# Performance work log

Measured on AMD Instinct MI355X. Metric: run time of the kernel, lower is better.

## Reference

```python
import jax, jax.numpy as jnp
import numpy as np
from jax.scipy.linalg import cholesky, solve_triangular, cho_solve

N, M, D = 16384, 2048, 8
VAR, LS = 1.0, 0.5      # RBF kernel hyperparameters (same for kernel_f and kernel_g)
JITTER = 1e-6
BATCH_RATE = 1.0
HALF_LOG_2PI = 0.5 * float(np.log(2.0 * np.pi))


def rbf(x1, x2):
    # K[i,j] = VAR * exp(-||x1_i - x2_j||^2 / (2 LS^2))
    d2 = (jnp.sum(x1 * x1, 1)[:, None] + jnp.sum(x2 * x2, 1)[None, :]
          - 2.0 * (x1 @ x2.T))
    return VAR * jnp.exp(-0.5 * d2 / (LS * LS))


def setup_inputs() -> dict:
    key = jax.random.key(0)
    ks = jax.random.split(key, 7)
    x = jax.random.normal(ks[0], (N, D), dtype=jnp.float32)
    y = jax.random.normal(ks[1], (N, 1), dtype=jnp.float32)
    z = 2.0 * jax.random.uniform(ks[2], (M, D), dtype=jnp.float32) - 1.0  # inducing inputs in [-1,1]^D
    q_m_f = 0.5 * jax.random.normal(ks[3], (M, 1), dtype=jnp.float32)
    q_m_g = 0.5 * jax.random.normal(ks[4], (M, 1), dtype=jnp.float32)
    # Cholesky-like params: identity plus small strictly-lower noise -> PD covariance
    q_L_f = jnp.eye(M, dtype=jnp.float32) + 0.01 * jnp.tril(
        jax.random.normal(ks[5], (M, M), dtype=jnp.float32), -1)
    q_L_g = jnp.eye(M, dtype=jnp.float32) + 0.01 * jnp.tril(
        jax.random.normal(ks[6], (M, M), dtype=jnp.float32), -1)
    return {"x": x, "y": y, "z": z, "q_m_f": q_m_f, "q_L_f": q_L_f,
            "q_m_g": q_m_g, "q_L_g": q_L_g}


def _gp_marginals_and_kl(x, z, q_m, q_L_raw):
    """Marginal posterior mean/var at x and KL(q(u)||p(u)) for one sparse GP."""
    L_S = jnp.tril(q_L_raw)                     # [M,M]
    Kuu = rbf(z, z) + JITTER * jnp.eye(M, dtype=x.dtype)
    Lk = cholesky(Kuu, lower=True)
    Kfu = rbf(x, z)                             # [N,M]
    # A = Kfu @ Kuu^{-1}
    A = cho_solve((Lk, True), Kfu.T).T          # [N,M]
    m = (A @ q_m)[:, 0]                         # [N]
    # diag(Kff + A (S - Kuu) A^T) = diag(Kff) + diag(A S A^T) - diag(Kfu A^T)
    S = L_S @ L_S.T
    diag_Kff = jnp.full((x.shape[0],), VAR, dtype=x.dtype)
    v = diag_Kff + jnp.sum((A @ S) * A, axis=1) - jnp.sum(A * Kfu, axis=1)
    # KL(N(q_m, S) || N(0, Kuu))
    alpha = solve_triangular(Lk, q_m, lower=True)       # Kuu^{-1/2} m
    W = solve_triangular(Lk, L_S, lower=True)           # Kuu^{-1/2} L_S
    logdet_K = 2.0 * jnp.sum(jnp.log(jnp.diag(Lk)))
    logdet_S = 2.0 * jnp.sum(jnp.log(jnp.abs(jnp.diag(L_S))))
    kl = 0.5 * (jnp.sum(W * W) + jnp.sum(alpha * alpha)
                - jnp.asarray(M, x.dtype) + logdet_K - logdet_S)
    return m, v, kl


def reference(x, y, z, q_m_f, q_L_f, q_m_g, q_L_g):
    m_f, v_f, kl_f = _gp_marginals_and_kl(x, z, q_m_f, q_L_f)
    m_g, v_g, kl_g = _gp_marginals_and_kl(x, z, q_m_g, q_L_g)
    yv = y[:, 0]
    # HetGaussian variational expectation (Saul et al. 2016):
    # E_q[log N(y | f, exp(g))] per point
    expectation = (-HALF_LOG_2PI - 0.5 * m_g
                   - 0.5 * ((yv - m_f) ** 2 + v_f) * jnp.exp(-m_g + 0.5 * v_g))
    elbo = BATCH_RATE * jnp.sum(expectation) - (kl_f + kl_g)
    return -elbo
```

## Files before the change

kernel.cpp:

```cpp
#include <hip/hip_runtime.h>
#include <math.h>

#define NN 16384
#define MM 2048
#define DD 8
#define NB 32
#define GRIDN 512
#define SZB ((size_t)16777216)

constexpr float HLOG2PI = 0.91893853320467274178f;

using short8  = __attribute__((ext_vector_type(8))) short;
using float4v = __attribute__((ext_vector_type(4))) float;

__device__ __forceinline__ float4v f4zero(){ float4v v; v[0]=0.f; v[1]=0.f; v[2]=0.f; v[3]=0.f; return v; }

__device__ __forceinline__ void bfsplit(float v, short& h, short& lo){
  unsigned b = __float_as_uint(v);
  h = (short)(b >> 16);
  float hf = __uint_as_float(b & 0xFFFF0000u);
  lo = (short)(__float_as_uint(v - hf) >> 16);
}
__device__ __forceinline__ float bf2f(short s){
  return __uint_as_float(((unsigned)(unsigned short)s) << 16);
}
__device__ __forceinline__ float4v mfma3(short8 ah, short8 al, short8 bh, short8 bl, float4v c){
  c = __builtin_amdgcn_mfma_f32_16x16x32_bf16(ah, bh, c, 0, 0, 0);
  c = __builtin_amdgcn_mfma_f32_16x16x32_bf16(ah, bl, c, 0, 0, 0);
  c = __builtin_amdgcn_mfma_f32_16x16x32_bf16(al, bh, c, 0, 0, 0);
  return c;
}

__device__ __forceinline__ void gbar0(int* cnt, int* flag, int& gen){
  __syncthreads();
  if (threadIdx.x == 0){
    ++gen;
    __builtin_amdgcn_fence(__ATOMIC_RELEASE, "agent");
    int old = __hip_atomic_fetch_add(cnt, 1, __ATOMIC_RELAXED, __HIP_MEMORY_SCOPE_AGENT);
    if (old == gen*GRIDN - 1){
      __builtin_amdgcn_fence(__ATOMIC_ACQ_REL, "agent");
      __hip_atomic_store(flag, gen, __ATOMIC_RELAXED, __HIP_MEMORY_SCOPE_AGENT);
    } else {
      while (__hip_atomic_load(flag, __ATOMIC_RELAXED, __HIP_MEMORY_SCOPE_AGENT) < gen)
        __builtin_amdgcn_s_sleep(8);
    }
    __builtin_amdgcn_fence(__ATOMIC_ACQUIRE, "agent");
  }
  __syncthreads();
}

__device__ __forceinline__ void gbar_h(int* bar, int xcc, int myN, int nxcd, int& gen){
  __syncthreads();
  if (threadIdx.x == 0){
    ++gen;
    int* lcnt  = bar + xcc*32;
    int* lflag = bar + 512 + xcc*32;
    int* gcnt  = bar + 1024;
    int* gflag = bar + 1056;
    int old = __hip_atomic_fetch_add(lcnt, 1, __ATOMIC_RELAXED, __HIP_MEMORY_SCOPE_AGENT);
    if (old == gen*myN - 1){
      __builtin_amdgcn_fence(__ATOMIC_RELEASE, "agent");
      int g = __hip_atomic_fetch_add(gcnt, 1, __ATOMIC_RELAXED, __HIP_MEMORY_SCOPE_AGENT);
      if (g == gen*nxcd - 1){
        __hip_atomic_store(gflag, gen, __ATOMIC_RELAXED, __HIP_MEMORY_SCOPE_AGENT);
      } else {
        while (__hip_atomic_load(gflag, __ATOMIC_RELAXED, __HIP_MEMORY_SCOPE_AGENT) < gen)
          __builtin_amdgcn_s_sleep(8);
      }
      __builtin_amdgcn_fence(__ATOMIC_ACQUIRE, "agent");
      __hip_atomic_store(lflag, gen, __ATOMIC_RELAXED, __HIP_MEMORY_SCOPE_AGENT);
    } else {
      while (__hip_atomic_load(lflag, __ATOMIC_RELAXED, __HIP_MEMORY_SCOPE_AGENT) < gen)
        __builtin_amdgcn_s_sleep(8);
      __builtin_amdgcn_fence(__ATOMIC_ACQUIRE, "agent");
    }
  }
  __syncthreads();
}

__device__ __forceinline__ float block_reduce(float v, float* scratch){
  int lane = threadIdx.x & 63;
  int w    = threadIdx.x >> 6;
  #pragma unroll
  for (int off=32; off; off>>=1) v += __shfl_down(v, off, 64);
  __syncthreads();
  if (lane==0) scratch[w] = v;
  __syncthreads();
  float r = 0.f;
  if (threadIdx.x < 4) r = scratch[threadIdx.x];
  if (w==0){ r += __shfl_down(r, 2, 64); r += __shfl_down(r, 1, 64); }
  return r;
}

__device__ __forceinline__ void stage64(float (*S)[68], const float* __restrict__ g, int ld, int t){
  #pragma unroll
  for (int p=t; p<1024; p+=256)
    *(float4*)&S[p>>4][(p&15)*4] = *(const float4*)&g[(size_t)(p>>4)*ld + (p&15)*4];
}
__device__ __forceinline__ void tile_gemm_step(float acc[4][4], const float (*As)[68], const float (*Bs)[68], int tx, int ty){
  for (int k=0;k<64;++k){
    float ar[4], bc4[4];
    #pragma unroll
    for (int u=0;u<4;++u){ ar[u]=As[ty*4+u][k]; bc4[u]=Bs[k][tx*4+u]; }
    #pragma unroll
    for (int u=0;u<4;++u)
      #pragma unroll
      for (int v=0;v<4;++v) acc[u][v] += ar[u]*bc4[v];
  }
}
__device__ __forceinline__ void tile_syrk_step(float acc[4][4], const float (*P)[68], const float (*Q)[68], int tx, int ty){
  for (int k=0;k<64;++k){
    float pr[4], qc[4];
    #pragma unroll
    for (int u=0;u<4;++u){ pr[u]=P[ty*4+u][k]; qc[u]=Q[tx*4+u][k]; }
    #pragma unroll
    for (int u=0;u<4;++u)
      #pragma unroll
      for (int v=0;v<4;++v) acc[u][v] += pr[u]*qc[v];
  }
}

__device__ __forceinline__ void factor64_reg(const float (*S)[68],
    float* __restrict__ lkd, float* __restrict__ sdg_, int d, int t){
  if (t < 64){
    float xr[64];
    #pragma unroll
    for (int c4=0;c4<16;++c4) *(float4*)&xr[c4*4] = *(const float4*)&S[t][c4*4];
    float myrp = 1.f;
    #pragma unroll
    for (int j=0;j<64;++j){
      float ajj = __shfl(xr[j], j, 64);
      float piv = sqrtf(fmaxf(ajj, 1e-20f));
      float rp  = 1.f/piv;
      float val = xr[j]*rp;
      if (t==j){ xr[j] = piv; myrp = rp; }
      else if (t>j) xr[j] = val;
      else val = 0.f;
      #pragma unroll
      for (int c=j+1;c<64;++c){
        float vc = __shfl(val, c, 64);
        if (c<=t) xr[c] -= val*vc;
      }
    }
    #pragma unroll
    for (int c=0;c<64;++c) if (c>t) xr[c] = 0.f;
    #pragma unroll
    for (int c4=0;c4<16;++c4)
      *(float4*)&lkd[d*4096 + t*64 + c4*4] = *(float4*)&xr[c4*4];
    sdg_[d*64 + t] = myrp;
  }
}

__global__ __launch_bounds__(256, 2) void factor_coop(
    const float* __restrict__ z,
    const float* __restrict__ qlf, const float* __restrict__ qlg,
    const float* __restrict__ qmf, const float* __restrict__ qmg,
    float* __restrict__ kuu, float* __restrict__ linv,
    float* __restrict__ wf, float* __restrict__ wg,
    float* __restrict__ af, float* __restrict__ ag,
    float* __restrict__ ptmp, float* __restrict__ lkdiag,
    float* __restrict__ sdg, float* __restrict__ ltri, int* __restrict__ bar)
{
  __shared__ float As[64][68];
  __shared__ float Bs[64][68];
  __shared__ float Cs[64][68];
  __shared__ float sd[64];
  __shared__ int binfo[2];
  const int bid = blockIdx.x, t = threadIdx.x;
  const int tx = t & 15, ty = t >> 4;

  int xcc_r;
  asm volatile("s_getreg_b32 %0, hwreg(HW_REG_XCC_ID)" : "=s"(xcc_r));
  const int xcc = xcc_r & 15;
  if (t == 0)
    __hip_atomic_fetch_add(bar + 1152 + xcc*32, 1, __ATOMIC_RELAXED, __HIP_MEMORY_SCOPE_AGENT);
  int gen0 = 0;
  gbar0(bar + 1088, bar + 1120, gen0);
  if (t == 0){
    int myN = __hip_atomic_load(bar + 1152 + xcc*32, __ATOMIC_RELAXED, __HIP_MEMORY_SCOPE_AGENT);
    int nx = 0;
    for (int i=0;i<16;++i)
      nx += (__hip_atomic_load(bar + 1152 + i*32, __ATOMIC_RELAXED, __HIP_MEMORY_SCOPE_AGENT) > 0);
    binfo[0] = myN; binfo[1] = nx;
  }
  __syncthreads();
  const int myN = binfo[0], nxcd = binfo[1];
  int gen = 0;

  if (bid == 0){
    for (int p=t; p<128; p+=256){ int i=p>>1, h=p&1;
      *(float4*)&As[i][h*4] = *(const float4*)&z[(size_t)i*DD + h*4]; }
    __syncthreads();
    float kv[4][4];
    #pragma unroll
    for (int u=0;u<4;++u)
      #pragma unroll
      for (int v=0;v<4;++v){
        float d2=0.f;
        #pragma unroll
        for (int d=0;d<8;++d){ float df=As[ty*4+u][d]-As[tx*4+v][d]; d2+=df*df; }
        kv[u][v] = __expf(-2.f*d2) + ((ty*4+u)==(tx*4+v) ? 1e-6f : 0.f);
      }
    __syncthreads();
    #pragma unroll
    for (int u=0;u<4;++u)
      #pragma unroll
      for (int v=0;v<4;++v) As[ty*4+u][tx*4+v] = kv[u][v];
    __syncthreads();
    factor64_reg(As, lkdiag, sdg, 0, t);
  } else {
    for (int idx=bid; idx<528; idx+=GRIDN-1){
      int r=0; while ((r+1)*(r+2)/2 <= idx) ++r;
      int c = idx - r*(r+1)/2;
      __syncthreads();
      for (int p=t; p<128; p+=256){ int i=p>>1, h=p&1;
        *(float4*)&As[i][h*4] = *(const float4*)&z[(size_t)(r*64+i)*DD + h*4];
        *(float4*)&Bs[i][h*4] = *(const float4*)&z[(size_t)(c*64+i)*DD + h*4]; }
      __syncthreads();
      #pragma unroll
      for (int u=0;u<4;++u){
        float4 o;
        float* ov = (float*)&o;
        #pragma unroll
        for (int v=0;v<4;++v){
          float d2=0.f;
          #pragma unroll
          for (int d=0;d<8;++d){ float df=As[ty*4+u][d]-Bs[tx*4+v][d]; d2+=df*df; }
          float val = __expf(-2.f*d2);
          if (r*64+ty*4+u == c*64+tx*4+v) val += 1e-6f;
          ov[v] = val;
        }
        *(float4*)&kuu[(size_t)(r*64+ty*4+u)*MM + c*64 + tx*4] = o;
      }
    }
  }
  gbar_h(bar, xcc, myN, nxcd, gen);

  for (int kb=0; kb<31; ++kb){
    int T = NB-1 - kb;
    int ntiles = T*(T+1)/2;
    if (bid < ntiles){
      stage64(Cs, lkdiag + kb*4096, 64, t);
      if (t < 64) sd[t] = sdg[kb*64 + t];
    }
    for (int idx=bid; idx<ntiles; idx+=GRIDN){
      int r=0; while ((r+1)*(r+2)/2 <= idx) ++r;
      int c = idx - r*(r+1)/2;
      int bi = kb+1+r, bc = kb+1+c;
      __syncthreads();
      stage64(As, kuu + (size_t)(bi*64)*MM + kb*64, MM, t);
      if (bc != bi) stage64(Bs, kuu + (size_t)(bc*64)*MM + kb*64, MM, t);
      __syncthreads();
      {
        int w = t>>6, l = t&63;
        if (w==0 || (w==1 && bc!=bi)){
          float (*S)[68] = (w==0)? As : Bs;
          float xr[64];
          #pragma unroll
          for (int c4=0;c4<16;++c4) *(float4*)&xr[c4*4] = *(const float4*)&S[l][c4*4];
          #pragma unroll
          for (int j=0;j<64;++j){
            float xj = xr[j]*sd[j];
            xr[j] = xj;
            #pragma unroll
            for (int cc=j+1;cc<64;++cc) xr[cc] -= xj*Cs[cc][j];
          }
          #pragma unroll
          for (int c4=0;c4<16;++c4) *(float4*)&S[l][c4*4] = *(float4*)&xr[c4*4];
        }
      }
      __syncthreads();
      if (bc == kb+1){
        for (int p=t;p<1024;p+=256)
          *(float4*)&ltri[(size_t)(bi*64+(p>>4))*MM + kb*64 + (p&15)*4] =
              *(float4*)&As[p>>4][(p&15)*4];
      }
      float acc[4][4] = {};
      tile_syrk_step(acc, As, (bc==bi)? As : Bs, tx, ty);
      if (bi==kb+1 && bc==kb+1){
        __syncthreads();
        #pragma unroll
        for (int u=0;u<4;++u)
          #pragma unroll
          for (int v=0;v<4;++v) Bs[ty*4+u][tx*4+v] = acc[u][v];
        __syncthreads();
        for (int p=t;p<1024;p+=256){
          int i=p>>4, c4=p&15;
          float4 kv = *(const float4*)&kuu[(size_t)(bi*64+i)*MM + bi*64 + c4*4];
          float4 bv = *(float4*)&Bs[i][c4*4];
          float4 o; o.x=kv.x-bv.x; o.y=kv.y-bv.y; o.z=kv.z-bv.z; o.w=kv.w-bv.w;
          *(float4*)&As[i][c4*4] = o;
        }
        __syncthreads();
        factor64_reg(As, lkdiag, sdg, kb+1, t);
      } else {
        #pragma unroll
        for (int u=0;u<4;++u){
          float4* dst = (float4*)&kuu[(size_t)(bi*64+ty*4+u)*MM + bc*64 + tx*4];
          float4 o = *dst;
          o.x-=acc[u][0]; o.y-=acc[u][1]; o.z-=acc[u][2]; o.w-=acc[u][3];
          *dst = o;
        }
      }
    }
    gbar_h(bar, xcc, myN, nxcd, gen);
  }

  if (bid < NB){
    stage64(As, lkdiag + bid*4096, 64, t);
    __syncthreads();
    if (t < 64){
      for (int j=0;j<64;++j){
        float s = (j==t)?1.f:0.f;
        for (int k=t;k<j;++k) s -= As[j][k]*Bs[k][t];
        Bs[j][t] = (j>=t)? s/As[j][j] : 0.f;
      }
    }
    __syncthreads();
    for (int p=t;p<1024;p+=256){ int i=p>>4, c4=p&15;
      *(float4*)&linv[(size_t)(bid*64+i)*MM + bid*64 + c4*4] = *(float4*)&Bs[i][c4*4]; }
  }
  gbar_h(bar, xcc, myN, nxcd, gen);

  for (int idx=bid; idx<16; idx+=GRIDN){
    int m = idx;
    __syncthreads();
    stage64(As, ltri + (size_t)((2*m+1)*64)*MM + (2*m)*64, MM, t);
    stage64(Bs, linv + (size_t)((2*m)*64)*MM   + (2*m)*64, MM, t);
    __syncthreads();
    float acc[4][4]={};
    tile_gemm_step(acc, As, Bs, tx, ty);
    __syncthreads();
    #pragma unroll
    for (int u=0;u<4;++u)
      #pragma unroll
      for (int v=0;v<4;++v) Bs[ty*4+u][tx*4+v] = acc[u][v];
    stage64(As, linv + (size_t)((2*m+1)*64)*MM + (2*m+1)*64, MM, t);
    __syncthreads();
    float o[4][4]={};
    tile_gemm_step(o, As, Bs, tx, ty);
    #pragma unroll
    for (int u=0;u<4;++u)
      *(float4*)&linv[(size_t)((2*m+1)*64+ty*4+u)*MM + (2*m)*64 + tx*4] =
          make_float4(-o[u][0],-o[u][1],-o[u][2],-o[u][3]);
  }
  gbar_h(bar, xcc, myN, nxcd, gen);

  for (int m=bid; m<8; m+=GRIDN){
    float* pm = ptmp + (size_t)m*128*128;
    for (int ti=0; ti<2; ++ti)
      for (int tj=0; tj<2; ++tj){
        int rb = m*4 + 2 + ti, cb0 = m*4;
        float acc[4][4]={};
        for (int k=tj; k<2; ++k){
          __syncthreads();
          stage64(As, ltri + (size_t)(rb*64)*MM + (cb0+k)*64, MM, t);
          stage64(Bs, linv + (size_t)((cb0+k)*64)*MM + (cb0+tj)*64, MM, t);
          __syncthreads();
          tile_gemm_step(acc, As, Bs, tx, ty);
        }
        #pragma unroll
        for (int u=0;u<4;++u)
          *(float4*)&pm[(size_t)(ti*64+ty*4+u)*128 + tj*64 + tx*4] =
              make_float4(acc[u][0],acc[u][1],acc[u][2],acc[u][3]);
      }
    for (int ti=0; ti<2; ++ti)
      for (int tj=0; tj<2; ++tj){
        int rb = m*4 + 2 + ti;
        float acc[4][4]={};
        for (int k=0; k<=ti; ++k){
          __syncthreads();
          stage64(As, linv + (size_t)(rb*64)*MM + (m*4+2+k)*64, MM, t);
          stage64(Bs, pm + (size_t)(k*64)*128 + tj*64, 128, t);
          __syncthreads();
          tile_gemm_step(acc, As, Bs, tx, ty);
        }
        #pragma unroll
        for (int u=0;u<4;++u)
          *(float4*)&linv[(size_t)(rb*64+ty*4+u)*MM + (m*4+tj)*64 + tx*4] =
              make_float4(-acc[u][0],-acc[u][1],-acc[u][2],-acc[u][3]);
      }
  }
  gbar_h(bar, xcc, myN, nxcd, gen);

  for (int s=2; s<5; ++s){
    int nb = 1<<s, mc = 16>>s, b = 64<<s;
    float* pmb = ptmp + (s==2 ? 131072 : (s==3 ? 393216 : 917504));
    int tiles = mc*nb*nb;
    for (int idx=bid; idx<tiles; idx+=GRIDN){
      int m = idx/(nb*nb), r2 = idx%(nb*nb);
      int ti = r2/nb, tj = r2%nb;
      int rb = m*2*nb + nb + ti, cb0 = m*2*nb;
      float acc[4][4]={};
      for (int k=tj; k<nb; ++k){
        __syncthreads();
        stage64(As, ltri + (size_t)(rb*64)*MM + (cb0+k)*64, MM, t);
        stage64(Bs, linv + (size_t)((cb0+k)*64)*MM + (cb0+tj)*64, MM, t);
        __syncthreads();
        tile_gemm_step(acc, As, Bs, tx, ty);
      }
      float* pm = pmb + (size_t)m*b*b;
      #pragma unroll
      for (int u=0;u<4;++u)
        *(float4*)&pm[(size_t)(ti*64+ty*4+u)*b + tj*64 + tx*4] =
            make_float4(acc[u][0],acc[u][1],acc[u][2],acc[u][3]);
    }
    gbar_h(bar, xcc, myN, nxcd, gen);
    for (int idx=bid; idx<tiles; idx+=GRIDN){
      int m = idx/(nb*nb), r2 = idx%(nb*nb);
      int ti = r2/nb, tj = r2%nb;
      int rb = m*2*nb + nb + ti;
      const float* pm = pmb + (size_t)m*b*b;
      float acc[4][4]={};
      for (int k=0; k<=ti; ++k){
        __syncthreads();
        stage64(As, linv + (size_t)(rb*64)*MM + (m*2*nb+nb+k)*64, MM, t);
        stage64(Bs, pm + (size_t)(k*64)*b + tj*64, b, t);
        __syncthreads();
        tile_gemm_step(acc, As, Bs, tx, ty);
      }
      #pragma unroll
      for (int u=0;u<4;++u)
        *(float4*)&linv[(size_t)(rb*64+ty*4+u)*MM + (m*2*nb+tj)*64 + tx*4] =
            make_float4(-acc[u][0],-acc[u][1],-acc[u][2],-acc[u][3]);
    }
    gbar_h(bar, xcc, myN, nxcd, gen);
  }

  for (int idx=bid; idx<2*528; idx+=GRIDN){
    int gp = idx/528, rem = idx%528;
    int bi=0; while ((bi+1)*(bi+2)/2 <= rem) ++bi;
    int bj = rem - bi*(bi+1)/2;
    const float* ql = gp ? qlg : qlf;
    float* w        = gp ? wg  : wf;
    float acc[4][4]={};
    for (int bk=bj; bk<=bi; ++bk){
      __syncthreads();
      stage64(As, linv + (size_t)(bi*64)*MM + bk*64, MM, t);
      stage64(Bs, ql   + (size_t)(bk*64)*MM + bj*64, MM, t);
      __syncthreads();
      if (bk==bj){
        for (int p=t;p<4096;p+=256){ int i=p>>6, c=p&63; if (i<c) Bs[i][c]=0.f; }
        __syncthreads();
      }
      tile_gemm_step(acc, As, Bs, tx, ty);
    }
    #pragma unroll
    for (int u=0;u<4;++u)
      *(float4*)&w[(size_t)(bi*64+ty*4+u)*MM + bj*64 + tx*4] =
          make_float4(acc[u][0],acc[u][1],acc[u][2],acc[u][3]);
  }
  {
    int gw = bid*4 + (t>>6), l = t&63;
    for (int job=gw; job<4096; job+=GRIDN*4){
      int gp = job>>11, r = job&2047;
      const float* qm = gp ? qmg : qmf;
      float s=0.f;
      for (int c=l; c<=r; c+=64) s += linv[(size_t)r*MM+c]*qm[c];
      #pragma unroll
      for (int off=32; off; off>>=1) s += __shfl_down(s, off, 64);
      if (l==0) (gp ? ag : af)[r] = s;
    }
  }
}


__global__ __launch_bounds__(256) void zfrag_kernel(const float* __restrict__ z,
    short* __restrict__ zfh, short* __restrict__ zfl, float* __restrict__ zn2){
  int zr = blockIdx.x*256 + threadIdx.x;
  float v[DD]; float s = 0.f;
  #pragma unroll
  for (int d=0; d<DD; ++d){ v[d] = z[zr*DD + d]; s += v[d]*v[d]; }
  zn2[zr] = s;
  size_t base = (size_t)(zr >> 4)*512 + (zr & 15)*32;
  #pragma unroll
  for (int k=0; k<32; ++k){
    short h = 0, lo = 0;
    if (k < DD) bfsplit(v[k], h, lo);
    zfh[base + k] = h; zfl[base + k] = lo;
  }
}

__global__ __launch_bounds__(256) void red_small(const float* __restrict__ lkd,
    const float* __restrict__ qlf, const float* __restrict__ qlg,
    const float* __restrict__ af, const float* __restrict__ ag,
    float* __restrict__ scal){
  __shared__ float scratch[4];
  float ldk=0, ldf=0, ldg=0, a2f=0, a2g=0;
  for (int i=threadIdx.x;i<MM;i+=256){
    int kb = i>>6, r = i&63;
    ldk += __logf(lkd[kb*4096 + r*64 + r]);
    ldf += __logf(fabsf(qlf[(size_t)i*MM+i]));
    ldg += __logf(fabsf(qlg[(size_t)i*MM+i]));
    float v = af[i]; a2f += v*v;
    v = ag[i];       a2g += v*v;
  }
  float r;
  r = block_reduce(ldk, scratch); if (threadIdx.x==0) scal[0] = 2.f*r;
  r = block_reduce(ldf, scratch); if (threadIdx.x==0) scal[1] = 2.f*r;
  r = block_reduce(ldg, scratch); if (threadIdx.x==0) scal[2] = 2.f*r;
  r = block_reduce(a2f, scratch); if (threadIdx.x==0) scal[3] = r;
  r = block_reduce(a2g, scratch); if (threadIdx.x==0) scal[4] = r;
}

__global__ __launch_bounds__(256) void redw_kernel(const float* __restrict__ wf,
    const float* __restrict__ wg, float* __restrict__ scal){
  __shared__ float scratch[4];
  size_t start  = (size_t)blockIdx.x*256 + threadIdx.x;
  size_t stride = (size_t)gridDim.x*256;
  float sf=0, sg=0;
  for (size_t p=start;p<(size_t)MM*MM;p+=stride){
    float v=wf[p]; sf += v*v;
    v=wg[p];       sg += v*v;
  }
  float r = block_reduce(sf, scratch);
  if (threadIdx.x==0) atomicAdd(&scal[5], r);
  r = block_reduce(sg, scratch);
  if (threadIdx.x==0) atomicAdd(&scal[6], r);
}

__global__ void kl_kernel(const float* __restrict__ scal, float* __restrict__ out){
  float klf = 0.5f*(scal[5] + scal[3] - (float)MM + scal[0] - scal[1]);
  float klg = 0.5f*(scal[6] + scal[4] - (float)MM + scal[0] - scal[2]);
  out[0] += klf + klg;
}

__global__ __launch_bounds__(256) void split_rowmajor(const float* __restrict__ src,
    short* __restrict__ dh, short* __restrict__ dl){
  int p = blockIdx.x*256 + threadIdx.x;
  int chunk = p >> 9, wi = p & 511;
  int mo = chunk >> 6, ko = chunk & 63;
  int row = mo*16 + (wi >> 5), col = ko*32 + (wi & 31);
  float v = src[(size_t)row*MM + col];
  short h, lo; bfsplit(v, h, lo);
  dh[p] = h; dl[p] = lo;
}

__global__ __launch_bounds__(256) void split_transpose(const float* __restrict__ src,
    short* __restrict__ dh, short* __restrict__ dl){
  __shared__ float tile[32][33];
  int t = threadIdx.x;
  int mb = blockIdx.x, kb = blockIdx.y;
  #pragma unroll
  for (int k=0;k<4;++k){
    int idx = t + k*256;
// ... 220 lines not shown
        bh[tm] = *(const short8*)&lBh[off];
        bl[tm] = *(const short8*)&lBl[off];
      }
      #pragma unroll
      for (int tn=0; tn<4; ++tn)
        #pragma unroll
        for (int tm=0; tm<4; ++tm)
          acc[tn][tm] = mfma3(ah[tn], al[tn], bh[tm], bl[tm], acc[tn][tm]);
    }
  }
  float rs[16];
  #pragma unroll
  for (int tn=0; tn<4; ++tn)
    #pragma unroll
    for (int r=0; r<4; ++r){
      float s = 0.f;
      #pragma unroll
      for (int tm=0; tm<4; ++tm){ float v = acc[tn][tm][r]; s += v*v; }
      rs[tn*4+r] = s;
    }
  #pragma unroll
  for (int off=8; off; off>>=1)
    #pragma unroll
    for (int k=0; k<16; ++k) rs[k] += __shfl_down(rs[k], off, 16);
  if (li == 0){
    #pragma unroll
    for (int tn=0; tn<4; ++tn)
      #pragma unroll
      for (int r=0; r<4; ++r){
        int n = istrip*128 + (w>>1)*64 + tn*16 + q*4 + r;
        atomicAdd(&vq[n], rs[tn*4+r]);
      }
  }
}

__global__ __launch_bounds__(256) void final_kernel(const float* __restrict__ y,
    const float* __restrict__ t2, const float* __restrict__ lf, const float* __restrict__ lg,
    const float* __restrict__ vfq, const float* __restrict__ vgq, float* __restrict__ out){
  __shared__ float scratch[4];
  int i = blockIdx.x*256 + threadIdx.x;
  float mf = lf[i], mg = lg[i];
  float vf = 1.f + vfq[i] - t2[i];
  float vg = 1.f + vgq[i] - t2[i];
  float dy = y[i] - mf;
  float e = -HLOG2PI - 0.5f*mg - 0.5f*(dy*dy + vf)*__expf(-mg + 0.5f*vg);
  float r = block_reduce(e, scratch);
  if (threadIdx.x==0) atomicAdd(out, -r);
}

extern "C" void kernel_launch(void* const* d_in, const int* in_sizes, int n_in,
                              void* d_out, int out_size, void* d_ws, size_t ws_size,
                              hipStream_t stream){
  (void)in_sizes; (void)n_in; (void)out_size; (void)ws_size;
  const float* x   = (const float*)d_in[0];
  const float* y   = (const float*)d_in[1];
  const float* z   = (const float*)d_in[2];
  const float* qmf = (const float*)d_in[3];
  const float* qlf = (const float*)d_in[4];
  const float* qmg = (const float*)d_in[5];
  const float* qlg = (const float*)d_in[6];
  float* out = (float*)d_out;
  char* Bw = (char*)d_ws;

  float* kuu  = (float*)Bw;
  float* linv = (float*)(Bw + SZB);
  float* wf   = (float*)(Bw + 2*SZB);
  float* wg   = (float*)(Bw + 3*SZB);
  short* lvh  = (short*)Bw;
  short* lvl  = (short*)(Bw + SZB/2);
  short* wfh  = (short*)(Bw + SZB);
  short* wfl  = (short*)(Bw + SZB + SZB/2);
  short* wgh  = (short*)(Bw + 2*SZB);
  short* wgl  = (short*)(Bw + 2*SZB + SZB/2);
  short* tth  = (short*)(Bw + 3*SZB);
  short* ttl  = (short*)(Bw + 3*SZB + (size_t)NN*MM*2);
  float* ltri   = (float*)(Bw + 4*SZB);
  float* ptmp   = (float*)(Bw + 5*SZB);
  float* lkdiag = (float*)(Bw + 5*SZB + (size_t)8388608);
  float* sdg    = (float*)(Bw + 5*SZB + (size_t)8388608 + (size_t)524288);
  float* sm   = (float*)(Bw + 3*SZB + (size_t)NN*MM*4);
  float* af = sm;          float* ag = af + MM;
  float* t2 = ag + MM;     float* lf = t2 + NN;   float* lg = lf + NN;
  float* vfq = lg + NN;    float* vgq = vfq + NN; float* scal = vgq + NN;
  int*   bar = (int*)(scal + 64);
  float* zn2 = scal + 64 + 2048;
  short* zfh = (short*)(zn2 + MM);
  short* zfl = zfh + MM*32;

  hipMemsetAsync(out, 0, sizeof(float), stream);
  hipMemsetAsync(vfq, 0, (size_t)(2*NN + 64 + 2048)*sizeof(float), stream);
  hipMemsetAsync(wf,  0, 2*SZB, stream);
  hipMemsetAsync(linv,0, SZB,   stream);

  zfrag_kernel<<<MM/256, 256, 0, stream>>>(z, zfh, zfl, zn2);

  factor_coop<<<GRIDN, 256, 0, stream>>>(z, qlf, qlg, qmf, qmg,
                                         kuu, linv, wf, wg, af, ag,
                                         ptmp, lkdiag, sdg, ltri, bar);

  red_small<<<1, 256, 0, stream>>>(lkdiag, qlf, qlg, af, ag, scal);
  redw_kernel<<<512, 256, 0, stream>>>(wf, wg, scal);
  kl_kernel<<<1, 1, 0, stream>>>(scal, out);

  split_rowmajor<<<MM*MM/256, 256, 0, stream>>>(linv, lvh, lvl);
  split_transpose<<<dim3(MM/32, MM/32), 256, 0, stream>>>(wf, wfh, wfl);
  split_transpose<<<dim3(MM/32, MM/32), 256, 0, stream>>>(wg, wgh, wgl);

  tt_mfma<<<dim3(NN/128, MM/128), 256, 0, stream>>>(x, zn2, zfh, zfl, lvh, lvl, tth, ttl);
  lin_v2<<<NN/4, 256, 0, stream>>>(tth, ttl, af, ag, t2, lf, lg);
  quad_mfma<<<dim3(NN/128, MM/128, 2), 256, 0, stream>>>(tth, ttl, wfh, wfl, wgh, wgl, vfq, vgq);
  final_kernel<<<NN/256, 256, 0, stream>>>(y, t2, lf, lg, vfq, vgq, out);
}
```

Measured before the change: 4.600 ms.

## Replace persistent cooperative factor kernel with per-phase kernel launches

Measured after the change: 3.914 ms. -14.9%, faster.

```diff
diff --git a/kernel.cpp b/kernel.cpp
--- a/kernel.cpp
+++ b/kernel.cpp
@@ -5,7 +5,6 @@
 #define MM 2048
 #define DD 8
 #define NB 32
-#define GRIDN 512
 #define SZB ((size_t)16777216)
 
 constexpr float HLOG2PI = 0.91893853320467274178f;
@@ -29,53 +28,6 @@
   c = __builtin_amdgcn_mfma_f32_16x16x32_bf16(ah, bl, c, 0, 0, 0);
   c = __builtin_amdgcn_mfma_f32_16x16x32_bf16(al, bh, c, 0, 0, 0);
   return c;
-}
-
-__device__ __forceinline__ void gbar0(int* cnt, int* flag, int& gen){
-  __syncthreads();
-  if (threadIdx.x == 0){
-    ++gen;
-    __builtin_amdgcn_fence(__ATOMIC_RELEASE, "agent");
-    int old = __hip_atomic_fetch_add(cnt, 1, __ATOMIC_RELAXED, __HIP_MEMORY_SCOPE_AGENT);
-    if (old == gen*GRIDN - 1){
-      __builtin_amdgcn_fence(__ATOMIC_ACQ_REL, "agent");
-      __hip_atomic_store(flag, gen, __ATOMIC_RELAXED, __HIP_MEMORY_SCOPE_AGENT);
-    } else {
-      while (__hip_atomic_load(flag, __ATOMIC_RELAXED, __HIP_MEMORY_SCOPE_AGENT) < gen)
-        __builtin_amdgcn_s_sleep(8);
-    }
-    __builtin_amdgcn_fence(__ATOMIC_ACQUIRE, "agent");
-  }
-  __syncthreads();
-}
-
-__device__ __forceinline__ void gbar_h(int* bar, int xcc, int myN, int nxcd, int& gen){
-  __syncthreads();
-  if (threadIdx.x == 0){
-    ++gen;
-    int* lcnt  = bar + xcc*32;
-    int* lflag = bar + 512 + xcc*32;
-    int* gcnt  = bar + 1024;
-    int* gflag = bar + 1056;
-    int old = __hip_atomic_fetch_add(lcnt, 1, __ATOMIC_RELAXED, __HIP_MEMORY_SCOPE_AGENT);
-    if (old == gen*myN - 1){
-      __builtin_amdgcn_fence(__ATOMIC_RELEASE, "agent");
-      int g = __hip_atomic_fetch_add(gcnt, 1, __ATOMIC_RELAXED, __HIP_MEMORY_SCOPE_AGENT);
-      if (g == gen*nxcd - 1){
-        __hip_atomic_store(gflag, gen, __ATOMIC_RELAXED, __HIP_MEMORY_SCOPE_AGENT);
-      } else {
-        while (__hip_atomic_load(gflag, __ATOMIC_RELAXED, __HIP_MEMORY_SCOPE_AGENT) < gen)
-          __builtin_amdgcn_s_sleep(8);
-      }
-      __builtin_amdgcn_fence(__ATOMIC_ACQUIRE, "agent");
-      __hip_atomic_store(lflag, gen, __ATOMIC_RELAXED, __HIP_MEMORY_SCOPE_AGENT);
-    } else {
-      while (__hip_atomic_load(lflag, __ATOMIC_RELAXED, __HIP_MEMORY_SCOPE_AGENT) < gen)
-        __builtin_amdgcn_s_sleep(8);
-      __builtin_amdgcn_fence(__ATOMIC_ACQUIRE, "agent");
-    }
-  }
-  __syncthreads();
 }
 
 __device__ __forceinline__ float block_reduce(float v, float* scratch){
@@ -151,316 +103,297 @@
   }
 }
 
-__global__ __launch_bounds__(256, 2) void factor_coop(
-    const float* __restrict__ z,
-    const float* __restrict__ qlf, const float* __restrict__ qlg,
-    const float* __restrict__ qmf, const float* __restrict__ qmg,
-    float* __restrict__ kuu, float* __restrict__ linv,
-    float* __restrict__ wf, float* __restrict__ wg,
-    float* __restrict__ af, float* __restrict__ ag,
-    float* __restrict__ ptmp, float* __restrict__ lkdiag,
-    float* __restrict__ sdg, float* __restrict__ ltri, int* __restrict__ bar)
-{
+
+__global__ __launch_bounds__(256) void phase0_kernel(
+    const float* __restrict__ z, float* __restrict__ kuu){
+  __shared__ float As[64][68];
+  __shared__ float Bs[64][68];
+  const int t = threadIdx.x, tx = t & 15, ty = t >> 4;
+  int idx = blockIdx.x;
+  int r=0; while ((r+1)*(r+2)/2 <= idx) ++r;
+  int c = idx - r*(r+1)/2;
+  for (int p=t; p<128; p+=256){ int i=p>>1, h=p&1;
+    *(float4*)&As[i][h*4] = *(const float4*)&z[(size_t)(r*64+i)*DD + h*4];
+    *(float4*)&Bs[i][h*4] = *(const float4*)&z[(size_t)(c*64+i)*DD + h*4]; }
+  __syncthreads();
+  #pragma unroll
+  for (int u=0;u<4;++u){
+    float4 o;
+    float* ov = (float*)&o;
+    #pragma unroll
+    for (int v=0;v<4;++v){
+      float d2=0.f;
+      #pragma unroll
+      for (int d=0;d<8;++d){ float df=As[ty*4+u][d]-Bs[tx*4+v][d]; d2+=df*df; }
+      float val = __expf(-2.f*d2);
+      if (r*64+ty*4+u == c*64+tx*4+v) val += 1e-6f;
+      ov[v] = val;
+    }
+    *(float4*)&kuu[(size_t)(r*64+ty*4+u)*MM + c*64 + tx*4] = o;
+  }
+}
+
+__global__ __launch_bounds__(256) void diag0_kernel(
+    const float* __restrict__ kuu, float* __restrict__ lkdiag, float* __restrict__ sdg){
+  __shared__ float As[64][68];
+  const int t = threadIdx.x;
+  stage64(As, kuu, MM, t);
+  __syncthreads();
+  factor64_reg(As, lkdiag, sdg, 0, t);
+}
+
+__global__ __launch_bounds__(256) void panel_kernel(
+    float* __restrict__ kuu, float* __restrict__ lkdiag,
+    float* __restrict__ sdg, float* __restrict__ ltri, int kb){
   __shared__ float As[64][68];
   __shared__ float Bs[64][68];
   __shared__ float Cs[64][68];
   __shared__ float sd[64];
-  __shared__ int binfo[2];
-  const int bid = blockIdx.x, t = threadIdx.x;
-  const int tx = t & 15, ty = t >> 4;
-
-  int xcc_r;
-  asm volatile("s_getreg_b32 %0, hwreg(HW_REG_XCC_ID)" : "=s"(xcc_r));
-  const int xcc = xcc_r & 15;
-  if (t == 0)
-    __hip_atomic_fetch_add(bar + 1152 + xcc*32, 1, __ATOMIC_RELAXED, __HIP_MEMORY_SCOPE_AGENT);
-  int gen0 = 0;
-  gbar0(bar + 1088, bar + 1120, gen0);
-  if (t == 0){
-    int myN = __hip_atomic_load(bar + 1152 + xcc*32, __ATOMIC_RELAXED, __HIP_MEMORY_SCOPE_AGENT);
-    int nx = 0;
-    for (int i=0;i<16;++i)
-      nx += (__hip_atomic_load(bar + 1152 + i*32, __ATOMIC_RELAXED, __HIP_MEMORY_SCOPE_AGENT) > 0);
-    binfo[0] = myN; binfo[1] = nx;
-  }
-  __syncthreads();
-  const int myN = binfo[0], nxcd = binfo[1];
-  int gen = 0;
-
-  if (bid == 0){
-    for (int p=t; p<128; p+=256){ int i=p>>1, h=p&1;
-      *(float4*)&As[i][h*4] = *(const float4*)&z[(size_t)i*DD + h*4]; }
-    __syncthreads();
-    float kv[4][4];
+  const int t = threadIdx.x, tx = t & 15, ty = t >> 4;
+  int idx = blockIdx.x;
+  int r=0; while ((r+1)*(r+2)/2 <= idx) ++r;
+  int c = idx - r*(r+1)/2;
+  int bi = kb+1+r, bc = kb+1+c;
+  stage64(Cs, lkdiag + kb*4096, 64, t);
+  if (t < 64) sd[t] = sdg[kb*64 + t];
+  stage64(As, kuu + (size_t)(bi*64)*MM + kb*64, MM, t);
+  if (bc != bi) stage64(Bs, kuu + (size_t)(bc*64)*MM + kb*64, MM, t);
+  __syncthreads();
+  {
+    int w = t>>6, l = t&63;
+    if (w==0 || (w==1 && bc!=bi)){
+      float (*S)[68] = (w==0)? As : Bs;
+      float xr[64];
+      #pragma unroll
+      for (int c4=0;c4<16;++c4) *(float4*)&xr[c4*4] = *(const float4*)&S[l][c4*4];
+      #pragma unroll
+      for (int j=0;j<64;++j){
+        float xj = xr[j]*sd[j];
+        xr[j] = xj;
+        #pragma unroll
+        for (int cc=j+1;cc<64;++cc) xr[cc] -= xj*Cs[cc][j];
+      }
+      #pragma unroll
+      for (int c4=0;c4<16;++c4) *(float4*)&S[l][c4*4] = *(float4*)&xr[c4*4];
+    }
+  }
+  __syncthreads();
+  if (bc == kb+1){
+    for (int p=t;p<1024;p+=256)
+      *(float4*)&ltri[(size_t)(bi*64+(p>>4))*MM + kb*64 + (p&15)*4] =
+          *(float4*)&As[p>>4][(p&15)*4];
+  }
+  float acc[4][4] = {};
+  tile_syrk_step(acc, As, (bc==bi)? As : Bs, tx, ty);
+  if (bi==kb+1 && bc==kb+1){
+    __syncthreads();
     #pragma unroll
     for (int u=0;u<4;++u)
       #pragma unroll
-      for (int v=0;v<4;++v){
-        float d2=0.f;
-        #pragma unroll
-        for (int d=0;d<8;++d){ float df=As[ty*4+u][d]-As[tx*4+v][d]; d2+=df*df; }
-        kv[u][v] = __expf(-2.f*d2) + ((ty*4+u)==(tx*4+v) ? 1e-6f : 0.f);
-      }
-    __syncthreads();
-    #pragma unroll
-    for (int u=0;u<4;++u)
-      #pragma unroll
-      for (int v=0;v<4;++v) As[ty*4+u][tx*4+v] = kv[u][v];
-    __syncthreads();
-    factor64_reg(As, lkdiag, sdg, 0, t);
+      for (int v=0;v<4;++v) Bs[ty*4+u][tx*4+v] = acc[u][v];
+    __syncthreads();
+    for (int p=t;p<1024;p+=256){
+      int i=p>>4, c4=p&15;
+      float4 kv = *(const float4*)&kuu[(size_t)(bi*64+i)*MM + bi*64 + c4*4];
+      float4 bv = *(float4*)&Bs[i][c4*4];
+      float4 o; o.x=kv.x-bv.x; o.y=kv.y-bv.y; o.z=kv.z-bv.z; o.w=kv.w-bv.w;
+      *(float4*)&As[i][c4*4] = o;
+    }
+    __syncthreads();
+    factor64_reg(As, lkdiag, sdg, kb+1, t);
   } else {
-    for (int idx=bid; idx<528; idx+=GRIDN-1){
-      int r=0; while ((r+1)*(r+2)/2 <= idx) ++r;
-      int c = idx - r*(r+1)/2;
-      __syncthreads();
-      for (int p=t; p<128; p+=256){ int i=p>>1, h=p&1;
-        *(float4*)&As[i][h*4] = *(const float4*)&z[(size_t)(r*64+i)*DD + h*4];
-        *(float4*)&Bs[i][h*4] = *(const float4*)&z[(size_t)(c*64+i)*DD + h*4]; }
-      __syncthreads();
-      #pragma unroll
-      for (int u=0;u<4;++u){
-        float4 o;
-        float* ov = (float*)&o;
-        #pragma unroll
-        for (int v=0;v<4;++v){
-          float d2=0.f;
-          #pragma unroll
-          for (int d=0;d<8;++d){ float df=As[ty*4+u][d]-Bs[tx*4+v][d]; d2+=df*df; }
-          float val = __expf(-2.f*d2);
-          if (r*64+ty*4+u == c*64+tx*4+v) val += 1e-6f;
-          ov[v] = val;
-        }
-        *(float4*)&kuu[(size_t)(r*64+ty*4+u)*MM + c*64 + tx*4] = o;
-      }
-    }
-  }
-  gbar_h(bar, xcc, myN, nxcd, gen);
-
-  for (int kb=0; kb<31; ++kb){
-    int T = NB-1 - kb;
-    int ntiles = T*(T+1)/2;
-    if (bid < ntiles){
-      stage64(Cs, lkdiag + kb*4096, 64, t);
-      if (t < 64) sd[t] = sdg[kb*64 + t];
-    }
-    for (int idx=bid; idx<ntiles; idx+=GRIDN){
-      int r=0; while ((r+1)*(r+2)/2 <= idx) ++r;
-      int c = idx - r*(r+1)/2;
-      int bi = kb+1+r, bc = kb+1+c;
-      __syncthreads();
-      stage64(As, kuu + (size_t)(bi*64)*MM + kb*64, MM, t);
-      if (bc != bi) stage64(Bs, kuu + (size_t)(bc*64)*MM + kb*64, MM, t);
-      __syncthreads();
-      {
-        int w = t>>6, l = t&63;
-        if (w==0 || (w==1 && bc!=bi)){
-          float (*S)[68] = (w==0)? As : Bs;
-          float xr[64];
-          #pragma unroll
-          for (int c4=0;c4<16;++c4) *(float4*)&xr[c4*4] = *(const float4*)&S[l][c4*4];
-          #pragma unroll
-          for (int j=0;j<64;++j){
-            float xj = xr[j]*sd[j];
-            xr[j] = xj;
-            #pragma unroll
-            for (int cc=j+1;cc<64;++cc) xr[cc] -= xj*Cs[cc][j];
-          }
-          #pragma unroll
-          for (int c4=0;c4<16;++c4) *(float4*)&S[l][c4*4] = *(float4*)&xr[c4*4];
-        }
-      }
-      __syncthreads();
-      if (bc == kb+1){
-        for (int p=t;p<1024;p+=256)
-          *(float4*)&ltri[(size_t)(bi*64+(p>>4))*MM + kb*64 + (p&15)*4] =
-              *(float4*)&As[p>>4][(p&15)*4];
-      }
-      float acc[4][4] = {};
-      tile_syrk_step(acc, As, (bc==bi)? As : Bs, tx, ty);
-      if (bi==kb+1 && bc==kb+1){
-        __syncthreads();
-        #pragma unroll
-        for (int u=0;u<4;++u)
-          #pragma unroll
-          for (int v=0;v<4;++v) Bs[ty*4+u][tx*4+v] = acc[u][v];
-        __syncthreads();
-        for (int p=t;p<1024;p+=256){
-          int i=p>>4, c4=p&15;
-          float4 kv = *(const float4*)&kuu[(size_t)(bi*64+i)*MM + bi*64 + c4*4];
-          float4 bv = *(float4*)&Bs[i][c4*4];
-          float4 o; o.x=kv.x-bv.x; o.y=kv.y-bv.y; o.z=kv.z-bv.z; o.w=kv.w-bv.w;
-          *(float4*)&As[i][c4*4] = o;
-        }
-        __syncthreads();
-        factor64_reg(As, lkdiag, sdg, kb+1, t);
-      } else {
-        #pragma unroll
-        for (int u=0;u<4;++u){
-          float4* dst = (float4*)&kuu[(size_t)(bi*64+ty*4+u)*MM + bc*64 + tx*4];
-          float4 o = *dst;
-          o.x-=acc[u][0]; o.y-=acc[u][1]; o.z-=acc[u][2]; o.w-=acc[u][3];
-          *dst = o;
-        }
-      }
-    }
-    gbar_h(bar, xcc, myN, nxcd, gen);
-  }
-
-  if (bid < NB){
-    stage64(As, lkdiag + bid*4096, 64, t);
-    __syncthreads();
-    if (t < 64){
-      for (int j=0;j<64;++j){
-        float s = (j==t)?1.f:0.f;
-        for (int k=t;k<j;++k) s -= As[j][k]*Bs[k][t];
-        Bs[j][t] = (j>=t)? s/As[j][j] : 0.f;
-      }
-    }
-    __syncthreads();
-    for (int p=t;p<1024;p+=256){ int i=p>>4, c4=p&15;
-      *(float4*)&linv[(size_t)(bid*64+i)*MM + bid*64 + c4*4] = *(float4*)&Bs[i][c4*4]; }
-  }
-  gbar_h(bar, xcc, myN, nxcd, gen);
-
-  for (int idx=bid; idx<16; idx+=GRIDN){
-    int m = idx;
-    __syncthreads();
-    stage64(As, ltri + (size_t)((2*m+1)*64)*MM + (2*m)*64, MM, t);
-    stage64(Bs, linv + (size_t)((2*m)*64)*MM   + (2*m)*64, MM, t);
-    __syncthreads();
-    float acc[4][4]={};
-    tile_gemm_step(acc, As, Bs, tx, ty);
-    __syncthreads();
-    #pragma unroll
-    for (int u=0;u<4;++u)
-      #pragma unroll
-      for (int v=0;v<4;++v) Bs[ty*4+u][tx*4+v] = acc[u][v];
-    stage64(As, linv + (size_t)((2*m+1)*64)*MM + (2*m+1)*64, MM, t);
-    __syncthreads();
-    float o[4][4]={};
-    tile_gemm_step(o, As, Bs, tx, ty);
-    #pragma unroll
-    for (int u=0;u<4;++u)
-      *(float4*)&linv[(size_t)((2*m+1)*64+ty*4+u)*MM + (2*m)*64 + tx*4] =
-          make_float4(-o[u][0],-o[u][1],-o[u][2],-o[u][3]);
-  }
-  gbar_h(bar, xcc, myN, nxcd, gen);
-
-  for (int m=bid; m<8; m+=GRIDN){
-    float* pm = ptmp + (size_t)m*128*128;
-    for (int ti=0; ti<2; ++ti)
-      for (int tj=0; tj<2; ++tj){
-        int rb = m*4 + 2 + ti, cb0 = m*4;
-        float acc[4][4]={};
-        for (int k=tj; k<2; ++k){
-          __syncthreads();
-          stage64(As, ltri + (size_t)(rb*64)*MM + (cb0+k)*64, MM, t);
-          stage64(Bs, linv + (size_t)((cb0+k)*64)*MM + (cb0+tj)*64, MM, t);
-          __syncthreads();
-          tile_gemm_step(acc, As, Bs, tx, ty);
-        }
-        #pragma unroll
-        for (int u=0;u<4;++u)
-          *(float4*)&pm[(size_t)(ti*64+ty*4+u)*128 + tj*64 + tx*4] =
-              make_float4(acc[u][0],acc[u][1],acc[u][2],acc[u][3]);
-      }
-    for (int ti=0; ti<2; ++ti)
-      for (int tj=0; tj<2; ++tj){
-        int rb = m*4 + 2 + ti;
-        float acc[4][4]={};
-        for (int k=0; k<=ti; ++k){
-          __syncthreads();
-          stage64(As, linv + (size_t)(rb*64)*MM + (m*4+2+k)*64, MM, t);
-          stage64(Bs, pm + (size_t)(k*64)*128 + tj*64, 128, t);
-          __syncthreads();
-          tile_gemm_step(acc, As, Bs, tx, ty);
-        }
-        #pragma unroll
-        for (int u=0;u<4;++u)
-          *(float4*)&linv[(size_t)(rb*64+ty*4+u)*MM + (m*4+tj)*64 + tx*4] =
-              make_float4(-acc[u][0],-acc[u][1],-acc[u][2],-acc[u][3]);
-      }
-  }
-  gbar_h(bar, xcc, myN, nxcd, gen);
-
-  for (int s=2; s<5; ++s){
-    int nb = 1<<s, mc = 16>>s, b = 64<<s;
-    float* pmb = ptmp + (s==2 ? 131072 : (s==3 ? 393216 : 917504));
-    int tiles = mc*nb*nb;
-    for (int idx=bid; idx<tiles; idx+=GRIDN){
-      int m = idx/(nb*nb), r2 = idx%(nb*nb);
-      int ti = r2/nb, tj = r2%nb;
-      int rb = m*2*nb + nb + ti, cb0 = m*2*nb;
+    #pragma unroll
+    for (int u=0;u<4;++u){
+      float4* dst = (float4*)&kuu[(size_t)(bi*64+ty*4+u)*MM + bc*64 + tx*4];
+      float4 o = *dst;
+      o.x-=acc[u][0]; o.y-=acc[u][1]; o.z-=acc[u][2]; o.w-=acc[u][3];
+      *dst = o;
+    }
+  }
+}
+
+__global__ __launch_bounds__(256) void phase2_kernel(
+    const float* __restrict__ lkdiag, float* __restrict__ linv){
+  __shared__ float As[64][68];
+  __shared__ float Bs[64][68];
+  const int t = threadIdx.x, bid = blockIdx.x;
+  stage64(As, lkdiag + bid*4096, 64, t);
+  __syncthreads();
+  if (t < 64){
+    for (int j=0;j<64;++j){
+      float s = (j==t)?1.f:0.f;
+      for (int k=t;k<j;++k) s -= As[j][k]*Bs[k][t];
+      Bs[j][t] = (j>=t)? s/As[j][j] : 0.f;
+    }
+  }
+  __syncthreads();
+  for (int p=t;p<1024;p+=256){ int i=p>>4, c4=p&15;
+    *(float4*)&linv[(size_t)(bid*64+i)*MM + bid*64 + c4*4] = *(float4*)&Bs[i][c4*4]; }
+}
+
+__global__ __launch_bounds__(256) void p3l0_kernel(
+    const float* __restrict__ ltri, float* __restrict__ linv){
+  __shared__ float As[64][68];
+  __shared__ float Bs[64][68];
+  const int t = threadIdx.x, tx = t & 15, ty = t >> 4;
+  int m = blockIdx.x;
+  stage64(As, ltri + (size_t)((2*m+1)*64)*MM + (2*m)*64, MM, t);
+  stage64(Bs, linv + (size_t)((2*m)*64)*MM   + (2*m)*64, MM, t);
+  __syncthreads();
+  float acc[4][4]={};
+  tile_gemm_step(acc, As, Bs, tx, ty);
+  __syncthreads();
+  #pragma unroll
+  for (int u=0;u<4;++u)
+    #pragma unroll
+    for (int v=0;v<4;++v) Bs[ty*4+u][tx*4+v] = acc[u][v];
+  stage64(As, linv + (size_t)((2*m+1)*64)*MM + (2*m+1)*64, MM, t);
+  __syncthreads();
+  float o[4][4]={};
+  tile_gemm_step(o, As, Bs, tx, ty);
+  #pragma unroll
+  for (int u=0;u<4;++u)
+    *(float4*)&linv[(size_t)((2*m+1)*64+ty*4+u)*MM + (2*m)*64 + tx*4] =
+        make_float4(-o[u][0],-o[u][1],-o[u][2],-o[u][3]);
+}
+
+__global__ __launch_bounds__(256) void p3l1_kernel(
+    const float* __restrict__ ltri, float* __restrict__ linv, float* __restrict__ ptmp){
+  __shared__ float As[64][68];
+  __shared__ float Bs[64][68];
+  const int t = threadIdx.x, tx = t & 15, ty = t >> 4;
+  int m = blockIdx.x;
+  float* pm = ptmp + (size_t)m*128*128;
+  for (int ti=0; ti<2; ++ti)
+    for (int tj=0; tj<2; ++tj){
+      int rb = m*4 + 2 + ti, cb0 = m*4;
       float acc[4][4]={};
-      for (int k=tj; k<nb; ++k){
+      for (int k=tj; k<2; ++k){
         __syncthreads();
         stage64(As, ltri + (size_t)(rb*64)*MM + (cb0+k)*64, MM, t);
         stage64(Bs, linv + (size_t)((cb0+k)*64)*MM + (cb0+tj)*64, MM, t);
         __syncthreads();
         tile_gemm_step(acc, As, Bs, tx, ty);
       }
-      float* pm = pmb + (size_t)m*b*b;
       #pragma unroll
       for (int u=0;u<4;++u)
-        *(float4*)&pm[(size_t)(ti*64+ty*4+u)*b + tj*64 + tx*4] =
+        *(float4*)&pm[(size_t)(ti*64+ty*4+u)*128 + tj*64 + tx*4] =
             make_float4(acc[u][0],acc[u][1],acc[u][2],acc[u][3]);
     }
-    gbar_h(bar, xcc, myN, nxcd, gen);
-    for (int idx=bid; idx<tiles; idx+=GRIDN){
-      int m = idx/(nb*nb), r2 = idx%(nb*nb);
-      int ti = r2/nb, tj = r2%nb;
-      int rb = m*2*nb + nb + ti;
-      const float* pm = pmb + (size_t)m*b*b;
+  for (int ti=0; ti<2; ++ti)
+    for (int tj=0; tj<2; ++tj){
+      int rb = m*4 + 2 + ti;
       float acc[4][4]={};
       for (int k=0; k<=ti; ++k){
         __syncthreads();
-        stage64(As, linv + (size_t)(rb*64)*MM + (m*2*nb+nb+k)*64, MM, t);
-        stage64(Bs, pm + (size_t)(k*64)*b + tj*64, b, t);
+        stage64(As, linv + (size_t)(rb*64)*MM + (m*4+2+k)*64, MM, t);
+        stage64(Bs, pm + (size_t)(k*64)*128 + tj*64, 128, t);
         __syncthreads();
         tile_gemm_step(acc, As, Bs, tx, ty);
       }
       #pragma unroll
       for (int u=0;u<4;++u)
-        *(float4*)&linv[(size_t)(rb*64+ty*4+u)*MM + (m*2*nb+tj)*64 + tx*4] =
+        *(float4*)&linv[(size_t)(rb*64+ty*4+u)*MM + (m*4+tj)*64 + tx*4] =
             make_float4(-acc[u][0],-acc[u][1],-acc[u][2],-acc[u][3]);
     }
-    gbar_h(bar, xcc, myN, nxcd, gen);
-  }
-
-  for (int idx=bid; idx<2*528; idx+=GRIDN){
-    int gp = idx/528, rem = idx%528;
-    int bi=0; while ((bi+1)*(bi+2)/2 <= rem) ++bi;
-    int bj = rem - bi*(bi+1)/2;
-    const float* ql = gp ? qlg : qlf;
-    float* w        = gp ? wg  : wf;
-    float acc[4][4]={};
-    for (int bk=bj; bk<=bi; ++bk){
+}
+
+__global__ __launch_bounds__(256) void p3lA_kernel(
+    const float* __restrict__ ltri, const float* __restrict__ linv,
+    float* __restrict__ ptmp, int s){
+  __shared__ float As[64][68];
+  __shared__ float Bs[64][68];
+  const int t = threadIdx.x, tx = t & 15, ty = t >> 4;
+  int nb = 1<<s, b = 64<<s;
+  float* pmb = ptmp + (s==2 ? 131072 : (s==3 ? 393216 : 917504));
+  int idx = blockIdx.x;
+  int m = idx/(nb*nb), r2 = idx%(nb*nb);
+  int ti = r2/nb, tj = r2%nb;
+  int rb = m*2*nb + nb + ti, cb0 = m*2*nb;
+  float acc[4][4]={};
+  for (int k=tj; k<nb; ++k){
+    __syncthreads();
+    stage64(As, ltri + (size_t)(rb*64)*MM + (cb0+k)*64, MM, t);
+    stage64(Bs, linv + (size_t)((cb0+k)*64)*MM + (cb0+tj)*64, MM, t);
+    __syncthreads();
+    tile_gemm_step(acc, As, Bs, tx, ty);
+  }
+  float* pm = pmb + (size_t)m*b*b;
+  #pragma unroll
+  for (int u=0;u<4;++u)
+    *(float4*)&pm[(size_t)(ti*64+ty*4+u)*b + tj*64 + tx*4] =
+        make_float4(acc[u][0],acc[u][1],acc[u][2],acc[u][3]);
+}
+
+__global__ __launch_bounds__(256) void p3lB_kernel(
+    float* __restrict__ linv, const float* __restrict__ ptmp, int s){
+  __shared__ float As[64][68];
+  __shared__ float Bs[64][68];
+  const int t = threadIdx.x, tx = t & 15, ty = t >> 4;
+  int nb = 1<<s, b = 64<<s;
+  const float* pmb = ptmp + (s==2 ? 131072 : (s==3 ? 393216 : 917504));
+  int idx = blockIdx.x;
+  int m = idx/(nb*nb), r2 = idx%(nb*nb);
+  int ti = r2/nb, tj = r2%nb;
+  int rb = m*2*nb + nb + ti;
+  const float* pm = pmb + (size_t)m*b*b;
+  float acc[4][4]={};
+  for (int k=0; k<=ti; ++k){
+    __syncthreads();
+    stage64(As, linv + (size_t)(rb*64)*MM + (m*2*nb+nb+k)*64, MM, t);
+    stage64(Bs, pm + (size_t)(k*64)*b + tj*64, b, t);
+    __syncthreads();
+    tile_gemm_step(acc, As, Bs, tx, ty);
+  }
+  #pragma unroll
+  for (int u=0;u<4;++u)
+    *(float4*)&linv[(size_t)(rb*64+ty*4+u)*MM + (m*2*nb+tj)*64 + tx*4] =
+        make_float4(-acc[u][0],-acc[u][1],-acc[u][2],-acc[u][3]);
+}
+
+__global__ __launch_bounds__(256) void w_kernel(
+    const float* __restrict__ linv, const float* __restrict__ qlf,
+    const float* __restrict__ qlg, float* __restrict__ wf, float* __restrict__ wg){
+  __shared__ float As[64][68];
+  __shared__ float Bs[64][68];
+  const int t = threadIdx.x, tx = t & 15, ty = t >> 4;
+  int idx = blockIdx.x;
+  int gp = idx/528, rem = idx%528;
+  int bi=0; while ((bi+1)*(bi+2)/2 <= rem) ++bi;
+  int bj = rem - bi*(bi+1)/2;
+  const float* ql = gp ? qlg : qlf;
+  float* w        = gp ? wg  : wf;
+  float acc[4][4]={};
+  for (int bk=bj; bk<=bi; ++bk){
+    __syncthreads();
+    stage64(As, linv + (size_t)(bi*64)*MM + bk*64, MM, t);
+    stage64(Bs, ql   + (size_t)(bk*64)*MM + bj*64, MM, t);
+    __syncthreads();
+    if (bk==bj){
+      for (int p=t;p<4096;p+=256){ int i=p>>6, c=p&63; if (i<c) Bs[i][c]=0.f; }
       __syncthreads();
-      stage64(As, linv + (size_t)(bi*64)*MM + bk*64, MM, t);
-      stage64(Bs, ql   + (size_t)(bk*64)*MM + bj*64, MM, t);
-      __syncthreads();
-      if (bk==bj){
-        for (int p=t;p<4096;p+=256){ int i=p>>6, c=p&63; if (i<c) Bs[i][c]=0.f; }
-        __syncthreads();
-      }
-      tile_gemm_step(acc, As, Bs, tx, ty);
-    }
-    #pragma unroll
-    for (int u=0;u<4;++u)
-      *(float4*)&w[(size_t)(bi*64+ty*4+u)*MM + bj*64 + tx*4] =
-          make_float4(acc[u][0],acc[u][1],acc[u][2],acc[u][3]);
-  }
-  {
-    int gw = bid*4 + (t>>6), l = t&63;
-    for (int job=gw; job<4096; job+=GRIDN*4){
-      int gp = job>>11, r = job&2047;
-      const float* qm = gp ? qmg : qmf;
-      float s=0.f;
-      for (int c=l; c<=r; c+=64) s += linv[(size_t)r*MM+c]*qm[c];
-      #pragma unroll
-      for (int off=32; off; off>>=1) s += __shfl_down(s, off, 64);
-      if (l==0) (gp ? ag : af)[r] = s;
-    }
+    }
+    tile_gemm_step(acc, As, Bs, tx, ty);
+  }
+  #pragma unroll
+  for (int u=0;u<4;++u)
+    *(float4*)&w[(size_t)(bi*64+ty*4+u)*MM + bj*64 + tx*4] =
+        make_float4(acc[u][0],acc[u][1],acc[u][2],acc[u][3]);
+}
+
+__global__ __launch_bounds__(256) void alpha_kernel(
+    const float* __restrict__ linv, const float* __restrict__ qmf,
+    const float* __restrict__ qmg, float* __restrict__ af, float* __restrict__ ag){
+  int t = threadIdx.x;
+  int gw = blockIdx.x*4 + (t>>6), l = t&63;
+  for (int job=gw; job<4096; job+=1024){
+    int gp = job>>11, r = job&2047;
+    const float* qm = gp ? qmg : qmf;
+    float s=0.f;
+    for (int c=l; c<=r; c+=64) s += linv[(size_t)r*MM+c]*qm[c];
+    #pragma unroll
+    for (int off=32; off; off>>=1) s += __shfl_down(s, off, 64);
+    if (l==0) (gp ? ag : af)[r] = s;
   }
 }
 
@@ -847,7 +780,6 @@
   float* af = sm;          float* ag = af + MM;
   float* t2 = ag + MM;     float* lf = t2 + NN;   float* lg = lf + NN;
   float* vfq = lg + NN;    float* vgq = vfq + NN; float* scal = vgq + NN;
-  int*   bar = (int*)(scal + 64);
   float* zn2 = scal + 64 + 2048;
   short* zfh = (short*)(zn2 + MM);
   short* zfl = zfh + MM*32;
@@ -859,9 +791,22 @@
 
   zfrag_kernel<<<MM/256, 256, 0, stream>>>(z, zfh, zfl, zn2);
 
-  factor_coop<<<GRIDN, 256, 0, stream>>>(z, qlf, qlg, qmf, qmg,
-                                         kuu, linv, wf, wg, af, ag,
-                                         ptmp, lkdiag, sdg, ltri, bar);
+  phase0_kernel<<<528, 256, 0, stream>>>(z, kuu);
+  diag0_kernel<<<1, 256, 0, stream>>>(kuu, lkdiag, sdg);
+  for (int kb = 0; kb < 31; ++kb){
+    int T = NB - 1 - kb;
+    panel_kernel<<<T*(T+1)/2, 256, 0, stream>>>(kuu, lkdiag, sdg, ltri, kb);
+  }
+  phase2_kernel<<<NB, 256, 0, stream>>>(lkdiag, linv);
+  p3l0_kernel<<<16, 256, 0, stream>>>(ltri, linv);
+  p3l1_kernel<<<8, 256, 0, stream>>>(ltri, linv, ptmp);
+  for (int s = 2; s < 5; ++s){
+    int nb = 1<<s, mc = 16>>s;
+    p3lA_kernel<<<mc*nb*nb, 256, 0, stream>>>(ltri, linv, ptmp, s);
+    p3lB_kernel<<<mc*nb*nb, 256, 0, stream>>>(linv, ptmp, s);
+  }
+  w_kernel<<<2*528, 256, 0, stream>>>(linv, qlf, qlg, wf, wg);
+  alpha_kernel<<<256, 256, 0, stream>>>(linv, qmf, qmg, af, ag);
 
   red_small<<<1, 256, 0, stream>>>(lkdiag, qlf, qlg, af, ag, scal);
   redw_kernel<<<512, 256, 0, stream>>>(wf, wg, scal);
```
